# Kernel tuning notes

Hardware: AMD Instinct MI355X
Metric: run time of the kernel (lower is better)

The kernel has to match this reference:

```python
import math
import jax, jax.numpy as jnp
import numpy as np

B, T, D, H, FF, V = 1, 1024, 768, 12, 3072, 8192
HD = D // H  # 64
EPS = 1e-5


def _alibi_slopes(n_heads):
    def pow2_slopes(n):
        start = 2.0 ** (-(2.0 ** (-(math.log2(n) - 3))))
        return [start * (start ** i) for i in range(n)]
    if n_heads & (n_heads - 1) == 0:
        s = pow2_slopes(n_heads)
    else:
        c = 2 ** int(math.floor(math.log2(n_heads)))
        s = pow2_slopes(c)
        eb = 2.0 ** (-(2.0 ** (-(math.log2(2 * c) - 3))))
        s += [eb * (eb ** i) for i in range(n_heads - c)]
    return np.asarray(s[:n_heads], dtype=np.float32)


def _layernorm(x, w, b):
    mu = jnp.mean(x, axis=-1, keepdims=True)
    var = jnp.mean(jnp.square(x - mu), axis=-1, keepdims=True)
    return (x - mu) * jax.lax.rsqrt(var + EPS) * w + b


def setup_inputs() -> dict:
    key = jax.random.key(0)
    ks = jax.random.split(key, 16)
    inp = {
        'xt': jax.random.normal(ks[0], (B, T, D), jnp.float32),
        'xe': jax.random.normal(ks[1], (B, T, D), jnp.float32),
        'ln1_w': jnp.ones((D,), jnp.float32),
        'ln1_b': jnp.zeros((D,), jnp.float32),
        'qk_w': jax.random.normal(ks[2], (2 * D, D), jnp.float32) * 0.02,
        'qk_b': jnp.zeros((2 * D,), jnp.float32),
        'v_fact': jax.random.normal(ks[3], (H, H), jnp.float32) * 0.02,
        'out_fact': jax.random.normal(ks[4], (H, H), jnp.float32) * 0.02,
        'ln2_w': jnp.ones((D,), jnp.float32),
        'ln2_b': jnp.zeros((D,), jnp.float32),
        # per-head DictFFN params, stacked with leading head axis
        'fc_w': jax.random.normal(ks[5], (H, FF, D), jnp.float32) * 0.02,
        'fc_b': jnp.zeros((H, FF), jnp.float32),
        'proj_w': jax.random.normal(ks[6], (H, HD, FF), jnp.float32) * 0.02,
        'proj_b': jnp.zeros((H, HD), jnp.float32),
        'dln_w': jnp.ones((H, HD), jnp.float32),
        'dln_b': jnp.zeros((H, HD), jnp.float32),
        'dict_emb': jax.random.normal(ks[7], (H, V, HD), jnp.float32) * 0.02,
    }
    return inp


def reference(xt, xe, ln1_w, ln1_b, qk_w, qk_b, v_fact, out_fact, ln2_w, ln2_b,
              fc_w, fc_b, proj_w, proj_b, dln_w, dln_b, dict_emb):
    slopes = jnp.asarray(_alibi_slopes(H))  # [H]

    # --- attention on ln1(xt + xe), values taken from raw xt ---
    x_norm = _layernorm(xt + xe, ln1_w, ln1_b)
    qk = x_norm @ qk_w.T + qk_b  # [B,T,2D]
    q, k = jnp.split(qk, 2, axis=-1)
    q = q.reshape(B, T, H, HD).transpose(0, 2, 1, 3)  # [B,H,T,hd]
    k = k.reshape(B, T, H, HD).transpose(0, 2, 1, 3)
    # Kronecker lift of v_fact == per-head mixing with identity blocks
    xt_heads = xt.reshape(B, T, H, HD)
    v = jnp.einsum('ij,btjd->bitd', v_fact, xt_heads)  # [B,H,T,hd]

    scale = 1.0 / math.sqrt(HD)
    scores = jnp.einsum('bhid,bhjd->bhij', q, k) * scale  # [B,H,T,T]
    pos = jnp.arange(T, dtype=jnp.float32)
    rel = pos[None, :] - pos[:, None]  # [T,T]
    bias = slopes[:, None, None] * rel[None, :, :]
    causal = jnp.tril(jnp.ones((T, T), bool))
    bias = jnp.where(causal[None], bias, -jnp.inf)
    attn = jax.nn.softmax(scores + bias[None], axis=-1)
    y = jnp.einsum('bhij,bhjd->bihd', attn, v)  # [B,T,H,hd]
    # output Kronecker lift: per-head mixing
    y = jnp.einsum('ij,btjd->btid', out_fact, y).reshape(B, T, D)
    xt_new = xt + y

    # --- per-head DictFFN on ln2(xt_new + xe) ---
    x2 = _layernorm(xt_new + xe, ln2_w, ln2_b)  # [B,T,D]
    h = jnp.einsum('btd,hfd->bhtf', x2, fc_w) + fc_b[None, :, None, :]
    h = jax.nn.gelu(h, approximate=False)
    h = jnp.einsum('bhtf,hef->bhte', h, proj_w) + proj_b[None, :, None, :]
    x_hat = _layernorm(h, dln_w[None, :, None, :], dln_b[None, :, None, :])  # [B,H,T,hd]
    dict_logits = jnp.einsum('bhte,hve->bhtv', x_hat, dict_emb)  # [B,H,T,V]
    dict_weights = jax.nn.softmax(dict_logits, axis=-1)
    x_recon = jnp.einsum('bhtv,hve->bhte', dict_weights, dict_emb)  # [B,H,T,hd]
    # per-head MSE, summed then divided by n_heads == mean over all
    dict_loss = jnp.mean(jnp.square(x_hat - x_recon))
    xe_new = xe + x_recon.transpose(0, 2, 1, 3).reshape(B, T, D)
    return xt_new, xe_new, dict_weights, dict_loss
```

## Files before the change

kernel.cpp:

```cpp
#include <hip/hip_runtime.h>
#include <math.h>

#define T 1024
#define D 768
#define H 12
#define HD 64
#define FF 3072
#define V 8192
#define EPS 1e-5f

typedef float float4e __attribute__((ext_vector_type(4)));
typedef short short8 __attribute__((ext_vector_type(8)));

__device__ __forceinline__ unsigned short f2bf(float f) {
    unsigned int u = __float_as_uint(f);
    unsigned int r = u + 0x7fffu + ((u >> 16) & 1u);
    return (unsigned short)(r >> 16);
}
__device__ __forceinline__ int imin(int a, int b) { return a < b ? a : b; }

#define GLL16(g, l)                                                                        \
    __builtin_amdgcn_global_load_lds((const __attribute__((address_space(1))) void*)(g),   \
                                     (__attribute__((address_space(3))) void*)(l), 16, 0, 0)

__global__ void cvt_kernel(const float* __restrict__ in, unsigned short* __restrict__ out,
                           long long n) {
    long long i = ((long long)blockIdx.x * 256 + threadIdx.x) * 4;
    if (i + 3 < n) {
        float4e v = *(const float4e*)(in + i);
        out[i + 0] = f2bf(v[0]);
        out[i + 1] = f2bf(v[1]);
        out[i + 2] = f2bf(v[2]);
        out[i + 3] = f2bf(v[3]);
    }
}

__global__ void ln_kernel(const float* __restrict__ a, const float* __restrict__ b,
                          const float* __restrict__ w, const float* __restrict__ bias,
                          unsigned short* __restrict__ out) {
    int t = blockIdx.x;
    int tid = threadIdx.x;
    __shared__ float red[256];
    float x[3];
    float s = 0.f;
#pragma unroll
    for (int k = 0; k < 3; k++) {
        int d = tid + k * 256;
        x[k] = a[t * D + d] + b[t * D + d];
        s += x[k];
    }
    red[tid] = s; __syncthreads();
    for (int o = 128; o > 0; o >>= 1) { if (tid < o) red[tid] += red[tid + o]; __syncthreads(); }
    float mu = red[0] / (float)D;
    __syncthreads();
    float sq = 0.f;
#pragma unroll
    for (int k = 0; k < 3; k++) { float dx = x[k] - mu; sq += dx * dx; }
    red[tid] = sq; __syncthreads();
    for (int o = 128; o > 0; o >>= 1) { if (tid < o) red[tid] += red[tid + o]; __syncthreads(); }
    float rstd = rsqrtf(red[0] / (float)D + EPS);
#pragma unroll
    for (int k = 0; k < 3; k++) {
        int d = tid + k * 256;
        out[t * D + d] = f2bf((x[k] - mu) * rstd * w[d] + bias[d]);
    }
}

template <int AM, int BM, bool GELU_, bool CB, bool ATOM, bool BIAS>
__global__ __launch_bounds__(256, 2)
void mfma_gemm(const void* __restrict__ Av, const void* __restrict__ Bv,
               const float* __restrict__ bias, void* __restrict__ Cv,
               int M, int N, int K, int lda, int ldb, int ldc,
               long long sA, long long sB, long long sBias, long long sC,
               int nTiles, int kLen) {
    const int bz = blockIdx.z;
    const int nt = blockIdx.x % nTiles;
    const int kc = blockIdx.x / nTiles;
    const int m0 = blockIdx.y * 128;
    const int n0 = nt * 128;
    const int kBeg = kc * kLen, kEnd = kBeg + kLen;

    const int tid = threadIdx.x;
    const int lane = tid & 63;
    const int w = tid >> 6;
    const int wm = w >> 1, wn = w & 1;

    __shared__ __align__(16) unsigned short Asb[128 * 32];
    __shared__ __align__(16) unsigned short Bs[128 * 32];

    float4e acc[4][4];
#pragma unroll
    for (int i = 0; i < 4; i++)
#pragma unroll
        for (int j = 0; j < 4; j++) acc[i][j] = (float4e){0.f, 0.f, 0.f, 0.f};

    const int q = lane >> 4, r = lane & 15;

    for (int k0 = kBeg; k0 < kEnd; k0 += 32) {
        __syncthreads();
        if constexpr (AM == 1) {
            const unsigned short* Ab = (const unsigned short*)Av + (long long)bz * sA;
            int rowA = lane >> 2, kg = (lane & 3) * 8;
#pragma unroll
            for (int s = 0; s < 2; s++) {
                int seg = w * 2 + s;
                int rs = seg * 16 + rowA;
                const unsigned short* g = Ab + (long long)(m0 + rs) * lda + k0 + kg;
                GLL16(g, &Asb[seg * 512]);
            }
        } else {
            const float* Af = (const float*)Av + (long long)bz * sA;
            int row = tid >> 1, half = tid & 1;
            const float4e* p = (const float4e*)(Af + (long long)(m0 + row) * lda + k0 + half * 16);
            float4e v0 = p[0], v1 = p[1], v2 = p[2], v3 = p[3];
            short8 s0, s1;
#pragma unroll
            for (int e = 0; e < 4; e++) {
                s0[e] = (short)f2bf(v0[e]); s0[e + 4] = (short)f2bf(v1[e]);
                s1[e] = (short)f2bf(v2[e]); s1[e + 4] = (short)f2bf(v3[e]);
            }
            *(short8*)&Asb[row * 32 + half * 16] = s0;
            *(short8*)&Asb[row * 32 + half * 16 + 8] = s1;
        }
        if constexpr (BM == 1) {
            const unsigned short* Bb = (const unsigned short*)Bv + (long long)bz * sB;
            int rowA = lane >> 2, kg = (lane & 3) * 8;
#pragma unroll
            for (int s = 0; s < 2; s++) {
                int seg = w * 2 + s;
                int rs = imin(n0 + seg * 16 + rowA, N - 1);
                const unsigned short* g = Bb + (long long)rs * ldb + k0 + kg;
                GLL16(g, &Bs[seg * 512]);
            }
        } else if constexpr (BM == 0) {
            const float* Bf = (const float*)Bv + (long long)bz * sB;
            int row = tid >> 1, half = tid & 1;
            const float4e* p = (const float4e*)(Bf + (long long)(n0 + row) * ldb + k0 + half * 16);
            float4e v0 = p[0], v1 = p[1], v2 = p[2], v3 = p[3];
            short8 s0, s1;
#pragma unroll
            for (int e = 0; e < 4; e++) {
                s0[e] = (short)f2bf(v0[e]); s0[e + 4] = (short)f2bf(v1[e]);
                s1[e] = (short)f2bf(v2[e]); s1[e + 4] = (short)f2bf(v3[e]);
            }
            *(short8*)&Bs[row * 32 + half * 16] = s0;
            *(short8*)&Bs[row * 32 + half * 16 + 8] = s1;
        } else {
            const float* Bf = (const float*)Bv + (long long)bz * sB;
            int kk = tid >> 3, nn = (tid & 7) * 8;
            const float4e* p = (const float4e*)(Bf + (long long)(k0 + kk) * ldb + nn);
            float4e v0 = p[0], v1 = p[1];
#pragma unroll
            for (int e = 0; e < 4; e++) {
                Bs[(nn + e) * 32 + kk] = f2bf(v0[e]);
                Bs[(nn + 4 + e) * 32 + kk] = f2bf(v1[e]);
            }
        }
        __syncthreads();
        short8 af[4], bfr[4];
#pragma unroll
        for (int i = 0; i < 4; i++)
            af[i] = *(const short8*)&Asb[(wm * 64 + i * 16 + r) * 32 + q * 8];
#pragma unroll
        for (int j = 0; j < 4; j++)
            bfr[j] = *(const short8*)&Bs[(wn * 64 + j * 16 + r) * 32 + q * 8];
#pragma unroll
        for (int i = 0; i < 4; i++)
#pragma unroll
            for (int j = 0; j < 4; j++)
                acc[i][j] = __builtin_amdgcn_mfma_f32_16x16x32_bf16(af[i], bfr[j], acc[i][j], 0, 0, 0);
    }

    float* Cf = (float*)Cv + (long long)bz * sC;
    unsigned short* Cb = (unsigned short*)Cv + (long long)bz * sC;
    if (BIAS) bias += (long long)bz * sBias;
#pragma unroll
    for (int j = 0; j < 4; j++) {
        int n = n0 + wn * 64 + j * 16 + r;
        if (n >= N) continue;
        float bj = BIAS ? bias[n] : 0.f;
#pragma unroll
        for (int i = 0; i < 4; i++) {
            int mb = m0 + wm * 64 + i * 16 + q * 4;
#pragma unroll
            for (int rr = 0; rr < 4; rr++) {
                float v2 = acc[i][j][rr] + bj;
                if (GELU_) v2 = 0.5f * v2 * (1.0f + erff(v2 * 0.70710678118654752f));
                long long idx = (long long)(mb + rr) * ldc + n;
                if (ATOM) atomicAdd(&Cf[idx], v2);
                else if (CB) Cb[idx] = f2bf(v2);
                else Cf[idx] = v2;
            }
        }
    }
}

__global__ void vmix_kernel(const float* __restrict__ xt, const float* __restrict__ vf,
                            unsigned short* __restrict__ vt) {
    int t = blockIdx.x, tid = threadIdx.x;
    __shared__ float f[144];
    if (tid < 144) f[tid] = vf[tid];
    __syncthreads();
#pragma unroll
    for (int k = 0; k < 3; k++) {
        int o = tid + k * 256;
        int i = o >> 6, d = o & 63;
        float acc = 0.f;
#pragma unroll
        for (int j = 0; j < 12; j++) acc += f[i * 12 + j] * xt[t * D + j * 64 + d];
        vt[((long long)(i * 64 + d) << 10) + t] = f2bf(acc);
    }
}

__global__ __launch_bounds__(256)
void attn_mfma_kernel(const unsigned short* __restrict__ qkb,
                      const unsigned short* __restrict__ vtb,
                      float* __restrict__ y) {
    const int h = blockIdx.y;
    const int q0 = blockIdx.x * 64;
    const int tid = threadIdx.x;
    const int w = tid >> 6, lane = tid & 63;
    const int r = lane & 15, qg = lane >> 4;
    const int rowbase = q0 + w * 16;

    __shared__ __align__(16) unsigned short Ps[4][16 * 64];

    short8 aq0, aq1;
    {
        const unsigned short* qrow = qkb + (long long)(rowbase + r) * 1536 + h * 64 + qg * 8;
        aq0 = *(const short8*)(qrow);
        aq1 = *(const short8*)(qrow + 32);
    }
    const float slope = (h < 8) ? exp2f(-(float)(h + 1)) : exp2f(-0.5f * (float)(h - 7));
    const float scale = 0.125f;

    float m[4], l[4];
    float4e o[4];
#pragma unroll
    for (int i = 0; i < 4; i++) {
        m[i] = -INFINITY; l[i] = 0.f;
        o[i] = (float4e){0.f, 0.f, 0.f, 0.f};
    }

    const int jmax = rowbase + 15;
    for (int j0 = 0; j0 <= jmax; j0 += 64) {
        float4e s[4];
#pragma unroll
        for (int jt = 0; jt < 4; jt++) s[jt] = (float4e){0.f, 0.f, 0.f, 0.f};
#pragma unroll
        for (int jt = 0; jt < 4; jt++) {
            const unsigned short* krow =
                qkb + (long long)(j0 + jt * 16 + r) * 1536 + 768 + h * 64 + qg * 8;
            short8 bk0 = *(const short8*)(krow);
            short8 bk1 = *(const short8*)(krow + 32);
            s[jt] = __builtin_amdgcn_mfma_f32_16x16x32_bf16(aq0, bk0, s[jt], 0, 0, 0);
            s[jt] = __builtin_amdgcn_mfma_f32_16x16x32_bf16(aq1, bk1, s[jt], 0, 0, 0);
        }
#pragma unroll
        for (int reg = 0; reg < 4; reg++) {
            const int tq = rowbase + qg * 4 + reg;
            float pv[4];
            float best = -INFINITY;
#pragma unroll
            for (int jt = 0; jt < 4; jt++) {
                int j = j0 + jt * 16 + r;
                float sv = s[jt][reg] * scale + slope * (float)(j - tq);
                if (j > tq) sv = -INFINITY;
                pv[jt] = sv;
                best = fmaxf(best, sv);
            }
#pragma unroll
            for (int mk = 1; mk < 16; mk <<= 1) best = fmaxf(best, __shfl_xor(best, mk));
            float mn = fmaxf(m[reg], best);
            float f = expf(m[reg] - mn);
            m[reg] = mn;
            float ls = 0.f;
#pragma unroll
            for (int jt = 0; jt < 4; jt++) {
                float p = expf(pv[jt] - mn);
                ls += p;
                Ps[w][(qg * 4 + reg) * 64 + jt * 16 + r] = f2bf(p);
            }
#pragma unroll
            for (int mk = 1; mk < 16; mk <<= 1) ls += __shfl_xor(ls, mk);
            l[reg] = l[reg] * f + ls;
            o[0][reg] *= f; o[1][reg] *= f; o[2][reg] *= f; o[3][reg] *= f;
        }
        short8 ap0 = *(const short8*)&Ps[w][r * 64 + qg * 8];
        short8 ap1 = *(const short8*)&Ps[w][r * 64 + 32 + qg * 8];
#pragma unroll
        for (int dt = 0; dt < 4; dt++) {
            const unsigned short* vr =
                vtb + ((long long)(h * 64 + dt * 16 + r) << 10) + j0 + qg * 8;
            short8 bv0 = *(const short8*)(vr);
            short8 bv1 = *(const short8*)(vr + 32);
            o[dt] = __builtin_amdgcn_mfma_f32_16x16x32_bf16(ap0, bv0, o[dt], 0, 0, 0);
            o[dt] = __builtin_amdgcn_mfma_f32_16x16x32_bf16(ap1, bv1, o[dt], 0, 0, 0);
        }
    }
#pragma unroll
    for (int reg = 0; reg < 4; reg++) {
        float inv = 1.0f / l[reg];
        int t = rowbase + qg * 4 + reg;
#pragma unroll
        for (int dt = 0; dt < 4; dt++)
            y[(long long)t * D + h * 64 + dt * 16 + r] = o[dt][reg] * inv;
    }
}

__global__ void outmix_kernel(const float* __restrict__ xt, const float* __restrict__ y,
                              const float* __restrict__ of, float* __restrict__ out) {
    int t = blockIdx.x, tid = threadIdx.x;
    __shared__ float f[144];
    if (tid < 144) f[tid] = of[tid];
    __syncthreads();
#pragma unroll
    for (int k = 0; k < 3; k++) {
        int o = tid + k * 256;
        int i = o >> 6, d = o & 63;
        float acc = 0.f;
#pragma unroll
        for (int j = 0; j < 12; j++) acc += f[i * 12 + j] * y[t * D + j * 64 + d];
        out[t * D + o] = xt[t * D + o] + acc;
    }
}

__global__ void headln_kernel(const float* __restrict__ in, const float* __restrict__ pb,
                              const float* __restrict__ w, const float* __restrict__ b,
                              float* __restrict__ out) {
    int rrow = blockIdx.x;
    int lane = threadIdx.x;
    int h = rrow >> 10;
    float x = in[rrow * 64 + lane] + pb[h * 64 + lane];
    float s = x;
    for (int o = 32; o > 0; o >>= 1) s += __shfl_xor(s, o);
    float mu = s * (1.0f / 64.0f);
    float dx = x - mu;
    float qv = dx * dx;
    for (int o = 32; o > 0; o >>= 1) qv += __shfl_xor(qv, o);
    float rstd = rsqrtf(qv * (1.0f / 64.0f) + EPS);
    out[rrow * 64 + lane] = dx * rstd * w[h * 64 + lane] + b[h * 64 + lane];
}

__global__ void softmax_kernel(float* __restrict__ p) {
    long long row = blockIdx.x;
    float4e* x = (float4e*)(p + row * V);
    const int tid = threadIdx.x;
    const int w = tid >> 6;
    __shared__ float red[8];
    float4e v[8];
    float lm = -INFINITY;
#pragma unroll
    for (int k = 0; k < 8; k++) {
        v[k] = x[tid + k * 256];
        lm = fmaxf(lm, fmaxf(fmaxf(v[k][0], v[k][1]), fmaxf(v[k][2], v[k][3])));
    }
#pragma unroll
    for (int mk = 1; mk < 64; mk <<= 1) lm = fmaxf(lm, __shfl_xor(lm, mk));
    if ((tid & 63) == 0) red[w] = lm;
    __syncthreads();
    float m = fmaxf(fmaxf(red[0], red[1]), fmaxf(red[2], red[3]));
    float ls = 0.f;
#pragma unroll
    for (int k = 0; k < 8; k++) {
#pragma unroll
        for (int e = 0; e < 4; e++) { v[k][e] = expf(v[k][e] - m); ls += v[k][e]; }
    }
#pragma unroll
    for (int mk = 1; mk < 64; mk <<= 1) ls += __shfl_xor(ls, mk);
    if ((tid & 63) == 0) red[4 + w] = ls;
    __syncthreads();
    float inv = 1.0f / (red[4] + red[5] + red[6] + red[7]);
#pragma unroll
    for (int k = 0; k < 8; k++) {
        v[k][0] *= inv; v[k][1] *= inv; v[k][2] *= inv; v[k][3] *= inv;
        x[tid + k * 256] = v[k];
    }
}

__global__ void loss_xe_kernel(const float* __restrict__ xhat, const float* __restrict__ xrec,
                               const float* __restrict__ xe, float* __restrict__ out_xe,
                               float* __restrict__ loss) {
    int i = blockIdx.x * 256 + threadIdx.x;
    float a = xhat[i], r = xrec[i];
    float df = a - r;
    int h = i >> 16;
    int t = (i >> 6) & 1023;
    int dd = i & 63;
    int oe = t * D + h * 64 + dd;
    out_xe[oe] = xe[oe] + r;
    __shared__ float red[256];
    red[threadIdx.x] = df * df; __syncthreads();
    for (int o = 128; o > 0; o >>= 1) { if (threadIdx.x < o) red[threadIdx.x] += red[threadIdx.x + o]; __syncthreads(); }
    if (threadIdx.x == 0) atomicAdd(loss, red[0] * (1.0f / 786432.0f));
}

extern "C" void kernel_launch(void* const* d_in, const int* in_sizes, int n_in,
                              void* d_out, int out_size, void* d_ws, size_t ws_size,
                              hipStream_t stream) {
    const float* xt = (const float*)d_in[0];
    const float* xe = (const float*)d_in[1];
    const float* ln1_w = (const float*)d_in[2];
    const float* ln1_b = (const float*)d_in[3];
    const float* qk_w = (const float*)d_in[4];
    const float* qk_b = (const float*)d_in[5];
    const float* v_fact = (const float*)d_in[6];
    const float* out_fact = (const float*)d_in[7];
    const float* ln2_w = (const float*)d_in[8];
    const float* ln2_b = (const float*)d_in[9];
    const float* fc_w = (const float*)d_in[10];
    const float* fc_b = (const float*)d_in[11];
    const float* proj_w = (const float*)d_in[12];
    const float* proj_b = (const float*)d_in[13];
    const float* dln_w = (const float*)d_in[14];
    const float* dln_b = (const float*)d_in[15];
    const float* dict_emb = (const float*)d_in[16];

    float* out_xt = (float*)d_out;
    float* out_xe = out_xt + (long long)T * D;
    float* out_dw = out_xe + (long long)T * D;
    float* out_loss = out_dw + (long long)H * T * V;

    unsigned short* hbuf = (unsigned short*)out_dw;
    float* sc = out_dw + 18874368;
    unsigned short* fc_wb   = (unsigned short*)(sc);
    unsigned short* qk_wb   = (unsigned short*)(sc + 14155776);
    unsigned short* proj_wb = (unsigned short*)(sc + 14155776 + 589824);
    unsigned short* xnormb  = (unsigned short*)(sc + 15925248);
    unsigned short* x2b     = (unsigned short*)(sc + 16318464);
    float* qkbuf = sc + 16711680;
    float* vbuf  = sc + 18284544;
    float* ybuf  = sc + 19070976;
    float* hproj = sc + 19857408;
    float* xhat = (float*)d_ws;
    float* xrec = xhat + 786432;

    hipMemsetAsync(out_loss, 0, sizeof(float), stream);
    hipMemsetAsync(hproj, 0, 786432 * sizeof(float), stream);
    hipMemsetAsync(xrec, 0, 786432 * sizeof(float), stream);

    cvt_kernel<<<27648, 256, 0, stream>>>(fc_w, fc_wb, 28311552LL);
    cvt_kernel<<<1152, 256, 0, stream>>>(qk_w, qk_wb, 1179648LL);
    cvt_kernel<<<2304, 256, 0, stream>>>(proj_w, proj_wb, 2359296LL);

    ln_kernel<<<T, 256, 0, stream>>>(xt, xe, ln1_w, ln1_b, xnormb);
    vmix_kernel<<<T, 256, 0, stream>>>(xt, v_fact, (unsigned short*)vbuf);
    mfma_gemm<1, 1, false, true, false, true><<<dim3(12, 8, 1), 256, 0, stream>>>(
        xnormb, qk_wb, qk_b, qkbuf, 1024, 1536, 768, 768, 768, 1536,
        0, 0, 0, 0, 12, 768);
    attn_mfma_kernel<<<dim3(16, 12), 256, 0, stream>>>(
        (const unsigned short*)qkbuf, (const unsigned short*)vbuf, ybuf);
    outmix_kernel<<<T, 256, 0, stream>>>(xt, ybuf, out_fact, out_xt);
    ln_kernel<<<T, 256, 0, stream>>>(out_xt, xe, ln2_w, ln2_b, x2b);
    mfma_gemm<1, 1, true, true, false, true><<<dim3(24, 8, 12), 256, 0, stream>>>(
        x2b, fc_wb, fc_b, hbuf, 1024, 3072, 768, 768, 768, 3072,
        0, (long long)FF * D, FF, (long long)T * FF, 24, 768);
    mfma_gemm<1, 1, false, false, true, false><<<dim3(2, 8, 12), 256, 0, stream>>>(
        hbuf, proj_wb, nullptr, hproj, 1024, 64, 3072, 3072, 3072, 64,
        (long long)T * FF, (long long)HD * FF, 0, (long long)T * HD, 1, 1536);
    headln_kernel<<<H * T, 64, 0, stream>>>(hproj, proj_b, dln_w, dln_b, xhat);
    mfma_gemm<0, 0, false, false, false, false><<<dim3(64, 8, 12), 256, 0, stream>>>(
        xhat, dict_emb, nullptr, out_dw, 1024, 8192, 64, 64, 64, 8192,
        (long long)T * HD, (long long)V * HD, 0, (long long)T * V, 64, 64);
    softmax_kernel<<<H * T, 256, 0, stream>>>(out_dw);
    mfma_gemm<0, 2, false, false, true, false><<<dim3(4, 8, 12), 256, 0, stream>>>(
        out_dw, dict_emb, nullptr, xrec, 1024, 64, 8192, 8192, 64, 64,
        (long long)T * V, (long long)V * HD, 0, (long long)T * HD, 1, 2048);
    loss_xe_kernel<<<(H * T * HD) / 256, 256, 0, stream>>>(xhat, xrec, xe, out_xe, out_loss);
}
```

Measured before the change: 1.151 ms.

## Fuse dictionary logits GEMM with softmax using a two-pass recompute kernel

Replaces the separate dictionary-logits GEMM and the row softmax with one kernel. It computes bf16 MFMA logits against the dictionary, keeps online max and sum per row, then recomputes the logits and writes normalized probabilities directly. This removes writing the full fp32 logit tensor and reading it back for the softmax, at the cost of doing the logit GEMM twice. The grid is small (192 blocks) and dictionary tiles are read from global memory with no LDS staging, so latency and store coalescing may limit it. The dictionary is converted to bf16 in the workspace, or in the tail of the output buffer when the workspace is too small. In that fallback the last head reads fp32 and converts in the kernel, so the staged copy in the output tail is not overwritten while it is still needed.

```diff
diff --git a/kernel.cpp b/kernel.cpp
--- a/kernel.cpp
+++ b/kernel.cpp
@@ -342,39 +342,113 @@
     out[rrow * 64 + lane] = dx * rstd * w[h * 64 + lane] + b[h * 64 + lane];
 }
 
-__global__ void softmax_kernel(float* __restrict__ p) {
-    long long row = blockIdx.x;
-    float4e* x = (float4e*)(p + row * V);
+template <bool BF16B>
+__global__ __launch_bounds__(256)
+void dictsm_kernel(const float* __restrict__ xhat, const unsigned short* __restrict__ dbb,
+                   const float* __restrict__ dbf, float* __restrict__ p, int h0,
+                   long long dbStride, long long dfStride) {
+    const int h = h0 + blockIdx.y;
     const int tid = threadIdx.x;
-    const int w = tid >> 6;
-    __shared__ float red[8];
-    float4e v[8];
-    float lm = -INFINITY;
-#pragma unroll
-    for (int k = 0; k < 8; k++) {
-        v[k] = x[tid + k * 256];
-        lm = fmaxf(lm, fmaxf(fmaxf(v[k][0], v[k][1]), fmaxf(v[k][2], v[k][3])));
-    }
-#pragma unroll
-    for (int mk = 1; mk < 64; mk <<= 1) lm = fmaxf(lm, __shfl_xor(lm, mk));
-    if ((tid & 63) == 0) red[w] = lm;
-    __syncthreads();
-    float m = fmaxf(fmaxf(red[0], red[1]), fmaxf(red[2], red[3]));
-    float ls = 0.f;
-#pragma unroll
-    for (int k = 0; k < 8; k++) {
-#pragma unroll
-        for (int e = 0; e < 4; e++) { v[k][e] = expf(v[k][e] - m); ls += v[k][e]; }
-    }
-#pragma unroll
-    for (int mk = 1; mk < 64; mk <<= 1) ls += __shfl_xor(ls, mk);
-    if ((tid & 63) == 0) red[4 + w] = ls;
-    __syncthreads();
-    float inv = 1.0f / (red[4] + red[5] + red[6] + red[7]);
-#pragma unroll
-    for (int k = 0; k < 8; k++) {
-        v[k][0] *= inv; v[k][1] *= inv; v[k][2] *= inv; v[k][3] *= inv;
-        x[tid + k * 256] = v[k];
+    const int w = tid >> 6, lane = tid & 63;
+    const int r = lane & 15, qg = lane >> 4;
+    const int t0 = blockIdx.x * 64 + w * 16;
+
+    const unsigned short* db = BF16B ? (dbb + (long long)blockIdx.y * dbStride) : nullptr;
+    const float* df = BF16B ? nullptr : (dbf + (long long)blockIdx.y * dfStride);
+
+    short8 aq0, aq1;
+    {
+        const float* xr = xhat + ((long long)(h * 1024 + t0 + r)) * 64 + qg * 8;
+        float4e a0 = *(const float4e*)xr, a1 = *(const float4e*)(xr + 4);
+        float4e a2 = *(const float4e*)(xr + 32), a3 = *(const float4e*)(xr + 36);
+#pragma unroll
+        for (int e = 0; e < 4; e++) {
+            aq0[e] = (short)f2bf(a0[e]); aq0[e + 4] = (short)f2bf(a1[e]);
+            aq1[e] = (short)f2bf(a2[e]); aq1[e + 4] = (short)f2bf(a3[e]);
+        }
+    }
+
+    float m[4], l[4];
+#pragma unroll
+    for (int i = 0; i < 4; i++) { m[i] = -INFINITY; l[i] = 0.f; }
+
+    for (int v0 = 0; v0 < V; v0 += 64) {
+        float4e s[4];
+#pragma unroll
+        for (int jt = 0; jt < 4; jt++) s[jt] = (float4e){0.f, 0.f, 0.f, 0.f};
+#pragma unroll
+        for (int jt = 0; jt < 4; jt++) {
+            short8 b0, b1;
+            if constexpr (BF16B) {
+                const unsigned short* bp = db + (long long)(v0 + jt * 16 + r) * 64 + qg * 8;
+                b0 = *(const short8*)bp;
+                b1 = *(const short8*)(bp + 32);
+            } else {
+                const float* fp = df + (long long)(v0 + jt * 16 + r) * 64 + qg * 8;
+                float4e c0 = *(const float4e*)fp, c1 = *(const float4e*)(fp + 4);
+                float4e c2 = *(const float4e*)(fp + 32), c3 = *(const float4e*)(fp + 36);
+#pragma unroll
+                for (int e = 0; e < 4; e++) {
+                    b0[e] = (short)f2bf(c0[e]); b0[e + 4] = (short)f2bf(c1[e]);
+                    b1[e] = (short)f2bf(c2[e]); b1[e + 4] = (short)f2bf(c3[e]);
+                }
+            }
+            s[jt] = __builtin_amdgcn_mfma_f32_16x16x32_bf16(aq0, b0, s[jt], 0, 0, 0);
+            s[jt] = __builtin_amdgcn_mfma_f32_16x16x32_bf16(aq1, b1, s[jt], 0, 0, 0);
+        }
+#pragma unroll
+        for (int reg = 0; reg < 4; reg++) {
+            float x0 = s[0][reg], x1 = s[1][reg], x2 = s[2][reg], x3 = s[3][reg];
+            float mx = fmaxf(fmaxf(x0, x1), fmaxf(x2, x3));
+            float mn = fmaxf(m[reg], mx);
+            l[reg] = l[reg] * __expf(m[reg] - mn) +
+                     (__expf(x0 - mn) + __expf(x1 - mn)) + (__expf(x2 - mn) + __expf(x3 - mn));
+            m[reg] = mn;
+        }
+    }
+    float Mf[4], inv[4];
+#pragma unroll
+    for (int reg = 0; reg < 4; reg++) {
+        float M = m[reg];
+#pragma unroll
+        for (int mk = 1; mk < 16; mk <<= 1) M = fmaxf(M, __shfl_xor(M, mk));
+        float li = l[reg] * __expf(m[reg] - M);
+#pragma unroll
+        for (int mk = 1; mk < 16; mk <<= 1) li += __shfl_xor(li, mk);
+        Mf[reg] = M;
+        inv[reg] = 1.0f / li;
+    }
+    for (int v0 = 0; v0 < V; v0 += 64) {
+        float4e s[4];
+#pragma unroll
+        for (int jt = 0; jt < 4; jt++) s[jt] = (float4e){0.f, 0.f, 0.f, 0.f};
+#pragma unroll
+        for (int jt = 0; jt < 4; jt++) {
+            short8 b0, b1;
+            if constexpr (BF16B) {
+                const unsigned short* bp = db + (long long)(v0 + jt * 16 + r) * 64 + qg * 8;
+                b0 = *(const short8*)bp;
+                b1 = *(const short8*)(bp + 32);
+            } else {
+                const float* fp = df + (long long)(v0 + jt * 16 + r) * 64 + qg * 8;
+                float4e c0 = *(const float4e*)fp, c1 = *(const float4e*)(fp + 4);
+                float4e c2 = *(const float4e*)(fp + 32), c3 = *(const float4e*)(fp + 36);
+#pragma unroll
+                for (int e = 0; e < 4; e++) {
+                    b0[e] = (short)f2bf(c0[e]); b0[e + 4] = (short)f2bf(c1[e]);
+                    b1[e] = (short)f2bf(c2[e]); b1[e + 4] = (short)f2bf(c3[e]);
+                }
+            }
+            s[jt] = __builtin_amdgcn_mfma_f32_16x16x32_bf16(aq0, b0, s[jt], 0, 0, 0);
+            s[jt] = __builtin_amdgcn_mfma_f32_16x16x32_bf16(aq1, b1, s[jt], 0, 0, 0);
+        }
+#pragma unroll
+        for (int reg = 0; reg < 4; reg++) {
+            long long rowoff = ((long long)(h * 1024 + t0 + qg * 4 + reg)) * V + v0;
+#pragma unroll
+            for (int jt = 0; jt < 4; jt++)
+                p[rowoff + jt * 16 + r] = __expf(s[jt][reg] - Mf[reg]) * inv[reg];
+        }
     }
 }
 
@@ -435,6 +509,10 @@
     float* xhat = (float*)d_ws;
     float* xrec = xhat + 786432;
 
+    const bool bigws = ws_size >= (size_t)(1572864LL * 4 + 6291456LL * 2);
+    unsigned short* db_ws = (unsigned short*)(xrec + 786432);
+    unsigned short* db_main = (unsigned short*)(out_dw + 92274688LL);
+
     hipMemsetAsync(out_loss, 0, sizeof(float), stream);
     hipMemsetAsync(hproj, 0, 786432 * sizeof(float), stream);
     hipMemsetAsync(xrec, 0, 786432 * sizeof(float), stream);
@@ -442,6 +520,7 @@
     cvt_kernel<<<27648, 256, 0, stream>>>(fc_w, fc_wb, 28311552LL);
     cvt_kernel<<<1152, 256, 0, stream>>>(qk_w, qk_wb, 1179648LL);
     cvt_kernel<<<2304, 256, 0, stream>>>(proj_w, proj_wb, 2359296LL);
+    cvt_kernel<<<6144, 256, 0, stream>>>(dict_emb, bigws ? db_ws : db_main, 6291456LL);
 
     ln_kernel<<<T, 256, 0, stream>>>(xt, xe, ln1_w, ln1_b, xnormb);
     vmix_kernel<<<T, 256, 0, stream>>>(xt, v_fact, (unsigned short*)vbuf);
@@ -459,10 +538,15 @@
         hbuf, proj_wb, nullptr, hproj, 1024, 64, 3072, 3072, 3072, 64,
         (long long)T * FF, (long long)HD * FF, 0, (long long)T * HD, 1, 1536);
     headln_kernel<<<H * T, 64, 0, stream>>>(hproj, proj_b, dln_w, dln_b, xhat);
-    mfma_gemm<0, 0, false, false, false, false><<<dim3(64, 8, 12), 256, 0, stream>>>(
-        xhat, dict_emb, nullptr, out_dw, 1024, 8192, 64, 64, 64, 8192,
-        (long long)T * HD, (long long)V * HD, 0, (long long)T * V, 64, 64);
-    softmax_kernel<<<H * T, 256, 0, stream>>>(out_dw);
+    if (bigws) {
+        dictsm_kernel<true><<<dim3(16, 12), 256, 0, stream>>>(
+            xhat, db_ws, nullptr, out_dw, 0, 524288LL, 0LL);
+    } else {
+        dictsm_kernel<true><<<dim3(16, 11), 256, 0, stream>>>(
+            xhat, db_main, nullptr, out_dw, 0, 524288LL, 0LL);
+        dictsm_kernel<false><<<dim3(16, 1), 256, 0, stream>>>(
+            xhat, nullptr, dict_emb + 11LL * 524288, out_dw, 11, 0LL, 0LL);
+    }
     mfma_gemm<0, 2, false, false, true, false><<<dim3(4, 8, 12), 256, 0, stream>>>(
         out_dw, dict_emb, nullptr, xrec, 1024, 64, 8192, 8192, 64, 64,
         (long long)T * V, (long long)V * HD, 0, (long long)T * HD, 1, 2048);
```

Result: slower. 1.244 ms (+8.1%).
